# Optimization experiments

Measured on AMD Instinct MI355X. Metric: run time of the kernel, lower is better.

Reference implementation:

```python
import jax, jax.numpy as jnp
import numpy as np

B, N, E0, F_IN, H, EMB, VEC, DPI = 1024, 256, 2048, 6, 32, 32, 26, 512


def setup_inputs() -> dict:
    key = jax.random.key(0)
    ks = jax.random.split(key, 16)
    # fixed urban scene graph, shared by every batch element, with self-loops
    src0 = jax.random.randint(ks[0], (E0,), 0, N, dtype=jnp.int32)
    dst0 = jax.random.randint(ks[1], (E0,), 0, N, dtype=jnp.int32)
    loops = jnp.arange(N, dtype=jnp.int32)
    src = jnp.concatenate([src0, loops])
    dst = jnp.concatenate([dst0, loops])

    s = 0.05
    return {
        "graph_feats": jax.random.normal(ks[2], (B, N, F_IN), jnp.float32),
        "vector": jax.random.normal(ks[3], (B, VEC), jnp.float32),
        "src": src,
        "dst": dst,
        "W1": jax.random.normal(ks[4], (F_IN, H), jnp.float32) * s,
        "b1": jnp.zeros((H,), jnp.float32),
        "W2": jax.random.normal(ks[5], (H, H), jnp.float32) * s,
        "b2": jnp.zeros((H,), jnp.float32),
        "W3": jax.random.normal(ks[6], (H, H), jnp.float32) * s,
        "b3": jnp.zeros((H,), jnp.float32),
        "W_emb": jax.random.normal(ks[7], (H, EMB), jnp.float32) * s,
        "b_emb": jnp.zeros((EMB,), jnp.float32),
        "W_pi": jax.random.normal(ks[8], (VEC + EMB, DPI), jnp.float32) * s,
        "b_pi": jnp.zeros((DPI,), jnp.float32),
        "W_vf": jax.random.normal(ks[9], (VEC + EMB, DPI), jnp.float32) * s,
        "b_vf": jnp.zeros((DPI,), jnp.float32),
    }


def _edge_norm(src, dst, n_nodes):
    # DGL GraphConv norm='both': out_deg(src)^-1/2 * in_deg(dst)^-1/2
    ones = jnp.ones(src.shape[0], jnp.float32)
    deg_out = jax.ops.segment_sum(ones, src, num_segments=n_nodes)
    deg_in = jax.ops.segment_sum(ones, dst, num_segments=n_nodes)
    inv_o = jnp.where(deg_out > 0, deg_out ** -0.5, 0.0)
    inv_i = jnp.where(deg_in > 0, deg_in ** -0.5, 0.0)
    return inv_o[src] * inv_i[dst]  # [E]


def _gconv(h, src, dst, norm, W, b):
    # h: [B, N, F]; symmetric-normalized aggregation then linear (DGL GraphConv)
    msg = h[:, src, :] * norm[None, :, None]          # [B, E, F]
    agg = jnp.zeros_like(h).at[:, dst, :].add(msg)     # [B, N, F]
    return agg @ W + b


def reference(graph_feats, vector, src, dst, W1, b1, W2, b2, W3, b3,
              W_emb, b_emb, W_pi, b_pi, W_vf, b_vf):
    n_nodes = graph_feats.shape[1]
    norm = _edge_norm(src, dst, n_nodes)
    h = jax.nn.relu(_gconv(graph_feats, src, dst, norm, W1, b1))
    h = jax.nn.relu(_gconv(h, src, dst, norm, W2, b2))
    h = jax.nn.relu(_gconv(h, src, dst, norm, W3, b3))  # three_layers=True
    hg = jnp.mean(h, axis=1)                 # dgl.mean_nodes -> [B, H]
    emb = hg @ W_emb + b_emb                 # [B, EMB]
    comb = jnp.concatenate([vector[:, :26], emb], axis=1)  # [B, 58]
    pi = jax.nn.relu(comb @ W_pi + b_pi)
    vf = jax.nn.relu(comb @ W_vf + b_vf)
    return pi, vf
```

## Files before the change

kernel.cpp:

```cpp
#include <hip/hip_runtime.h>
#include <hip/hip_fp16.h>

#define B_    1024
#define N_    256
#define E_    2304
#define EPT_  9
#define FIN_  6
#define VEC_  26
#define HSTR_ 40

typedef _Float16 half8 __attribute__((ext_vector_type(8)));
typedef float    f32x4 __attribute__((ext_vector_type(4)));

__global__ __launch_bounds__(256) void fused_kernel(
    const float* __restrict__ gf,
    const float* __restrict__ vec,
    const int* __restrict__ src, const int* __restrict__ dst,
    const float* __restrict__ W1, const float* __restrict__ b1,
    const float* __restrict__ W2, const float* __restrict__ b2,
    const float* __restrict__ W3, const float* __restrict__ b3,
    const float* __restrict__ We, const float* __restrict__ be,
    const float* __restrict__ Wpi, const float* __restrict__ bpi,
    const float* __restrict__ Wvf, const float* __restrict__ bvf,
    float2* __restrict__ out)
{
    __shared__ __align__(16) __half hbuf[N_ * HSTR_];
    __shared__ unsigned int packedE[E_];
    __shared__ float part[8 * 33];
    __shared__ float hgl[32];
    __shared__ float comb[VEC_ + 32];
    __shared__ int   wsum[4];

    const int t = threadIdx.x;
    const int b = blockIdx.x;
    const int lane = t & 63, wv = t >> 6;

    int*   deg_o  = (int*)hbuf;
    int*   deg_i  = (int*)hbuf + 256;
    int*   scanA  = (int*)hbuf + 512;
    int*   cursor = (int*)hbuf + 768;
    int*   perm   = (int*)hbuf + 1024;
    float* inv_o  = (float*)hbuf + 1280;
    float* inv_i  = (float*)hbuf + 1536;
    int*   bcnt   = (int*)hbuf + 1792;
    int*   boff   = (int*)hbuf + 1856;

    deg_o[t] = 0; deg_i[t] = 0;
    if (t < 64) bcnt[t] = 0;
    __syncthreads();

    int sB[EPT_], dB[EPT_];
#pragma unroll
    for (int i = 0; i < EPT_; ++i) { int e = t + 256 * i; sB[i] = src[e]; dB[i] = dst[e]; }
#pragma unroll
    for (int i = 0; i < EPT_; ++i) { atomicAdd(&deg_o[sB[i]], 1); atomicAdd(&deg_i[dB[i]], 1); }
    __syncthreads();

    const int dI = deg_i[t];
    {
        int dO = deg_o[t];
        inv_o[t] = dO > 0 ? rsqrtf((float)dO) : 0.f;
        inv_i[t] = dI > 0 ? rsqrtf((float)dI) : 0.f;
    }
    int x = dI;
#pragma unroll
    for (int d = 1; d < 64; d <<= 1) {
        int y = __shfl_up(x, d, 64);
        if (lane >= d) x += y;
    }
    if (lane == 63) wsum[wv] = x;
    const int bucket = dI > 63 ? 63 : dI;
    atomicAdd(&bcnt[bucket], 1);
    __syncthreads();

    {
        int prefix = 0;
#pragma unroll
        for (int w = 0; w < 3; ++w) if (w < wv) prefix += wsum[w];
        int incl = x + prefix;
        scanA[t]  = incl;
        cursor[t] = incl - dI;
    }
    if (t < 64) {
        int c = bcnt[t], xx = c;
#pragma unroll
        for (int d = 1; d < 64; d <<= 1) {
            int y = __shfl_up(xx, d, 64);
            if (lane >= d) xx += y;
        }
        boff[t] = xx - c;
    }
    __syncthreads();

    { int pos = atomicAdd(&boff[bucket], 1); perm[pos] = t; }
#pragma unroll
    for (int i = 0; i < EPT_; ++i) {
        int s = sB[i], dd = dB[i];
        int pos = atomicAdd(&cursor[dd], 1);
        float nrm = inv_o[s] * inv_i[dd];
        unsigned short h = __half_as_ushort(__float2half(nrm));
        packedE[pos] = ((unsigned int)s << 16) | (unsigned int)h;
    }
    __syncthreads();

    const int node = perm[t];
    const int end  = scanA[node];
    const int beg  = end - deg_i[node];
    __syncthreads();

    {
        const float* g = gf + (size_t)b * (N_ * FIN_);
        for (int i = t; i < N_ * 8; i += 256) {
            int n = i >> 3, k = i & 7;
            hbuf[n * HSTR_ + k] = __float2half((k < FIN_) ? g[n * FIN_ + k] : 0.f);
        }
    }
    __syncthreads();

    const __half2 z2 = __float2half2_rn(0.f);

    {
        __half2 a2[4] = {z2, z2, z2, z2};
        for (int e = beg; e < end; ++e) {
            unsigned int u = packedE[e];
            __half2 w2 = __half2half2(__ushort_as_half((unsigned short)(u & 0xffffu)));
            union { float4 f4; __half2 h2[4]; } r;
            r.f4 = *(const float4*)&hbuf[(u >> 16) * HSTR_];
#pragma unroll
            for (int q = 0; q < 4; ++q) a2[q] = __hfma2(w2, r.h2[q], a2[q]);
        }
        float a[FIN_], o[32];
#pragma unroll
        for (int k = 0; k < FIN_; ++k)
            a[k] = (k & 1) ? __high2float(a2[k >> 1]) : __low2float(a2[k >> 1]);
#pragma unroll
        for (int j = 0; j < 32; ++j) o[j] = b1[j];
#pragma unroll
        for (int k = 0; k < FIN_; ++k) {
            float ak = a[k];
            const float* wr = &W1[k * 32];
#pragma unroll
            for (int j = 0; j < 32; ++j) o[j] += ak * wr[j];
        }
        __syncthreads();
        union { float4 f4; __half2 h2[4]; } w;
        float4* row = (float4*)&hbuf[node * HSTR_];
#pragma unroll
        for (int q = 0; q < 4; ++q) {
#pragma unroll
            for (int r = 0; r < 4; ++r)
                w.h2[r] = __floats2half2_rn(fmaxf(o[8*q + 2*r], 0.f), fmaxf(o[8*q + 2*r + 1], 0.f));
            row[q] = w.f4;
        }
    }
    __syncthreads();

    const int m16  = lane & 15;
    const int q4   = lane >> 4;
    const int slab = wv * 64;

    for (int L = 0; L < 2; ++L) {
        const float* Wl = (L == 0) ? W2 : W3;
        const float* Bl = (L == 0) ? b2 : b3;

        half8 bfrag[2];
        float bias_c[2];
#pragma unroll
        for (int h = 0; h < 2; ++h) {
            int col = m16 + 16 * h;
#pragma unroll
            for (int j = 0; j < 8; ++j)
                bfrag[h][j] = (_Float16)Wl[(q4 * 8 + j) * 32 + col];
            bias_c[h] = Bl[col];
        }

        __half2 acc2[16];
#pragma unroll
        for (int j = 0; j < 16; ++j) acc2[j] = z2;
        for (int e = beg; e < end; ++e) {
            unsigned int u = packedE[e];
            __half2 w2 = __half2half2(__ushort_as_half((unsigned short)(u & 0xffffu)));
            const float4* hr = (const float4*)&hbuf[(u >> 16) * HSTR_];
            union { float4 f4; __half2 h2[4]; } r0, r1, r2, r3;
            r0.f4 = hr[0]; r1.f4 = hr[1]; r2.f4 = hr[2]; r3.f4 = hr[3];
#pragma unroll
            for (int q = 0; q < 4; ++q) {
                acc2[q]      = __hfma2(w2, r0.h2[q], acc2[q]);
                acc2[4 + q]  = __hfma2(w2, r1.h2[q], acc2[4 + q]);
                acc2[8 + q]  = __hfma2(w2, r2.h2[q], acc2[8 + q]);
                acc2[12 + q] = __hfma2(w2, r3.h2[q], acc2[12 + q]);
            }
        }
        __syncthreads();
        {
            union { float4 f4; __half2 h2[4]; } w;
            float4* row = (float4*)&hbuf[node * HSTR_];
#pragma unroll
            for (int q = 0; q < 4; ++q) {
#pragma unroll
                for (int r = 0; r < 4; ++r) w.h2[r] = acc2[4 * q + r];
                row[q] = w.f4;
            }
        }
        __syncthreads();

        half8 afrag[4];
#pragma unroll
        for (int g = 0; g < 4; ++g) {
            union { float4 f4; half8 h8; } u;
            u.f4 = *(const float4*)&hbuf[(slab + g * 16 + m16) * HSTR_ + q4 * 8];
            afrag[g] = u.h8;
        }
        f32x4 D[4][2];
#pragma unroll
        for (int g = 0; g < 4; ++g) {
#pragma unroll
            for (int h = 0; h < 2; ++h) {
                f32x4 c = {bias_c[h], bias_c[h], bias_c[h], bias_c[h]};
                D[g][h] = __builtin_amdgcn_mfma_f32_16x16x32_f16(afrag[g], bfrag[h], c, 0, 0, 0);
            }
        }
#pragma unroll
        for (int g = 0; g < 4; ++g) {
#pragma unroll
            for (int h = 0; h < 2; ++h) {
#pragma unroll
                for (int r = 0; r < 4; ++r) {
                    float v = fmaxf(D[g][h][r], 0.f);
                    hbuf[(slab + g * 16 + q4 * 4 + r) * HSTR_ + h * 16 + m16] = __float2half(v);
                }
            }
        }
        __syncthreads();
    }

    {
        int j = t & 31, g8 = t >> 5;
        float s = 0.f;
        for (int i = 0; i < 32; ++i)
            s += __half2float(hbuf[(g8 * 32 + i) * HSTR_ + j]);
        part[g8 * 33 + j] = s;
    }
    __syncthreads();
    if (t < 32) {
        float sum = 0.f;
#pragma unroll
        for (int g8 = 0; g8 < 8; ++g8) sum += part[g8 * 33 + t];
        hgl[t] = sum * (1.0f / 256.0f);
    }
    __syncthreads();

    if (t < 32) {
        float v = be[t];
#pragma unroll
        for (int j = 0; j < 32; ++j) v += hgl[j] * We[j * 32 + t];
        comb[VEC_ + t] = v;
    }
    if (t < VEC_) comb[t] = vec[b * VEC_ + t];
    __syncthreads();

    {
        float p0 = bpi[2 * t], p1 = bpi[2 * t + 1];
        float v0 = bvf[2 * t], v1 = bvf[2 * t + 1];
        const float2* Wp = (const float2*)Wpi;
        const float2* Wv = (const float2*)Wvf;
        for (int k = 0; k < VEC_ + 32; ++k) {
            float c = comb[k];
            float2 a = Wp[k * 256 + t];
            p0 += c * a.x; p1 += c * a.y;
            float2 d = Wv[k * 256 + t];
            v0 += c * d.x; v1 += c * d.y;
        }
        out[b * 256 + t]          = make_float2(fmaxf(p0, 0.f), fmaxf(p1, 0.f));
        out[262144 + b * 256 + t] = make_float2(fmaxf(v0, 0.f), fmaxf(v1, 0.f));
    }
}

extern "C" void kernel_launch(void* const* d_in, const int* in_sizes, int n_in,
                              void* d_out, int out_size, void* d_ws, size_t ws_size,
                              hipStream_t stream)
{
    fused_kernel<<<B_, 256, 0, stream>>>(
        (const float*)d_in[0], (const float*)d_in[1],
        (const int*)d_in[2], (const int*)d_in[3],
        (const float*)d_in[4], (const float*)d_in[5],
        (const float*)d_in[6], (const float*)d_in[7],
        (const float*)d_in[8], (const float*)d_in[9],
        (const float*)d_in[10], (const float*)d_in[11],
        (const float*)d_in[12], (const float*)d_in[13],
        (const float*)d_in[14], (const float*)d_in[15],
        (float2*)d_out);
}
```

Before: 119.0 us.

## Split CSR build and MLP head into separate kernels around the GNN kernel

```diff
diff --git a/kernel.cpp b/kernel.cpp
--- a/kernel.cpp
+++ b/kernel.cpp
@@ -12,102 +12,109 @@
 typedef _Float16 half8 __attribute__((ext_vector_type(8)));
 typedef float    f32x4 __attribute__((ext_vector_type(4)));
 
+
+__global__ __launch_bounds__(256) void csr_kernel(
+    const int* __restrict__ src, const int* __restrict__ dst,
+    int4* __restrict__ nodeinfo, unsigned int* __restrict__ gpack)
+{
+    __shared__ int   deg_o[N_], deg_i[N_], scanA[N_], cursor[N_], perm[N_];
+    __shared__ float inv_o[N_], inv_i[N_];
+    __shared__ int   bcnt[64], boff[64], wsum[4];
+
+    const int t = threadIdx.x;
+    const int lane = t & 63, wv = t >> 6;
+
+    deg_o[t] = 0; deg_i[t] = 0;
+    if (t < 64) bcnt[t] = 0;
+    __syncthreads();
+
+    int sB[EPT_], dB[EPT_];
+#pragma unroll
+    for (int i = 0; i < EPT_; ++i) { int e = t + 256 * i; sB[i] = src[e]; dB[i] = dst[e]; }
+#pragma unroll
+    for (int i = 0; i < EPT_; ++i) { atomicAdd(&deg_o[sB[i]], 1); atomicAdd(&deg_i[dB[i]], 1); }
+    __syncthreads();
+
+    const int dI = deg_i[t];
+    {
+        int dO = deg_o[t];
+        inv_o[t] = dO > 0 ? rsqrtf((float)dO) : 0.f;
+        inv_i[t] = dI > 0 ? rsqrtf((float)dI) : 0.f;
+    }
+    int x = dI;
+#pragma unroll
+    for (int d = 1; d < 64; d <<= 1) {
+        int y = __shfl_up(x, d, 64);
+        if (lane >= d) x += y;
+    }
+    if (lane == 63) wsum[wv] = x;
+    const int bucket = dI > 63 ? 63 : dI;
+    atomicAdd(&bcnt[bucket], 1);
+    __syncthreads();
+
+    {
+        int prefix = 0;
+#pragma unroll
+        for (int w = 0; w < 3; ++w) if (w < wv) prefix += wsum[w];
+        int incl = x + prefix;
+        scanA[t]  = incl;
+        cursor[t] = incl - dI;
+    }
+    if (t < 64) {
+        int c = bcnt[t], xx = c;
+#pragma unroll
+        for (int d = 1; d < 64; d <<= 1) {
+            int y = __shfl_up(xx, d, 64);
+            if (lane >= d) xx += y;
+        }
+        boff[t] = xx - c;
+    }
+    __syncthreads();
+
+    { int pos = atomicAdd(&boff[bucket], 1); perm[pos] = t; }
+#pragma unroll
+    for (int i = 0; i < EPT_; ++i) {
+        int s = sB[i], dd = dB[i];
+        int pos = atomicAdd(&cursor[dd], 1);
+        float nrm = inv_o[s] * inv_i[dd];
+        unsigned short h = __half_as_ushort(__float2half(nrm));
+        gpack[pos] = ((unsigned int)s << 16) | (unsigned int)h;
+    }
+    __syncthreads();
+
+    {
+        int node = perm[t];
+        int end  = scanA[node];
+        int beg  = end - deg_i[node];
+        nodeinfo[t] = make_int4(node, beg, end, 0);
+    }
+}
+
 __global__ __launch_bounds__(256) void fused_kernel(
     const float* __restrict__ gf,
     const float* __restrict__ vec,
-    const int* __restrict__ src, const int* __restrict__ dst,
     const float* __restrict__ W1, const float* __restrict__ b1,
     const float* __restrict__ W2, const float* __restrict__ b2,
     const float* __restrict__ W3, const float* __restrict__ b3,
     const float* __restrict__ We, const float* __restrict__ be,
-    const float* __restrict__ Wpi, const float* __restrict__ bpi,
-    const float* __restrict__ Wvf, const float* __restrict__ bvf,
-    float2* __restrict__ out)
+    const int4* __restrict__ nodeinfo,
+    const unsigned int* __restrict__ gpack,
+    float* __restrict__ gcomb)
 {
     __shared__ __align__(16) __half hbuf[N_ * HSTR_];
     __shared__ unsigned int packedE[E_];
     __shared__ float part[8 * 33];
     __shared__ float hgl[32];
-    __shared__ float comb[VEC_ + 32];
-    __shared__ int   wsum[4];
 
     const int t = threadIdx.x;
     const int b = blockIdx.x;
-    const int lane = t & 63, wv = t >> 6;
-
-    int*   deg_o  = (int*)hbuf;
-    int*   deg_i  = (int*)hbuf + 256;
-    int*   scanA  = (int*)hbuf + 512;
-    int*   cursor = (int*)hbuf + 768;
-    int*   perm   = (int*)hbuf + 1024;
-    float* inv_o  = (float*)hbuf + 1280;
-    float* inv_i  = (float*)hbuf + 1536;
-    int*   bcnt   = (int*)hbuf + 1792;
-    int*   boff   = (int*)hbuf + 1856;
-
-    deg_o[t] = 0; deg_i[t] = 0;
-    if (t < 64) bcnt[t] = 0;
-    __syncthreads();
-
-    int sB[EPT_], dB[EPT_];
-#pragma unroll
-    for (int i = 0; i < EPT_; ++i) { int e = t + 256 * i; sB[i] = src[e]; dB[i] = dst[e]; }
-#pragma unroll
-    for (int i = 0; i < EPT_; ++i) { atomicAdd(&deg_o[sB[i]], 1); atomicAdd(&deg_i[dB[i]], 1); }
-    __syncthreads();
-
-    const int dI = deg_i[t];
-    {
-        int dO = deg_o[t];
-        inv_o[t] = dO > 0 ? rsqrtf((float)dO) : 0.f;
-        inv_i[t] = dI > 0 ? rsqrtf((float)dI) : 0.f;
-    }
-    int x = dI;
-#pragma unroll
-    for (int d = 1; d < 64; d <<= 1) {
-        int y = __shfl_up(x, d, 64);
-        if (lane >= d) x += y;
-    }
-    if (lane == 63) wsum[wv] = x;
-    const int bucket = dI > 63 ? 63 : dI;
-    atomicAdd(&bcnt[bucket], 1);
-    __syncthreads();
-
-    {
-        int prefix = 0;
-#pragma unroll
-        for (int w = 0; w < 3; ++w) if (w < wv) prefix += wsum[w];
-        int incl = x + prefix;
-        scanA[t]  = incl;
-        cursor[t] = incl - dI;
-    }
-    if (t < 64) {
-        int c = bcnt[t], xx = c;
-#pragma unroll
-        for (int d = 1; d < 64; d <<= 1) {
-            int y = __shfl_up(xx, d, 64);
-            if (lane >= d) xx += y;
-        }
-        boff[t] = xx - c;
-    }
-    __syncthreads();
-
-    { int pos = atomicAdd(&boff[bucket], 1); perm[pos] = t; }
-#pragma unroll
-    for (int i = 0; i < EPT_; ++i) {
-        int s = sB[i], dd = dB[i];
-        int pos = atomicAdd(&cursor[dd], 1);
-        float nrm = inv_o[s] * inv_i[dd];
-        unsigned short h = __half_as_ushort(__float2half(nrm));
-        packedE[pos] = ((unsigned int)s << 16) | (unsigned int)h;
-    }
-    __syncthreads();
-
-    const int node = perm[t];
-    const int end  = scanA[node];
-    const int beg  = end - deg_i[node];
-    __syncthreads();
-
+    const int lane = t & 63;
+
+    const int4 ni = nodeinfo[t];
+    const int node = ni.x, beg = ni.y, end = ni.z;
+
+#pragma unroll
+    for (int i = 0; i < EPT_; ++i) packedE[t + 256 * i] = gpack[t + 256 * i];
     {
         const float* g = gf + (size_t)b * (N_ * FIN_);
         for (int i = t; i < N_ * 8; i += 256) {
@@ -157,7 +164,7 @@
 
     const int m16  = lane & 15;
     const int q4   = lane >> 4;
-    const int slab = wv * 64;
+    const int slab = (t >> 6) * 64;
 
     for (int L = 0; L < 2; ++L) {
         const float* Wl = (L == 0) ? W2 : W3;
@@ -254,25 +261,46 @@
         float v = be[t];
 #pragma unroll
         for (int j = 0; j < 32; ++j) v += hgl[j] * We[j * 32 + t];
-        comb[VEC_ + t] = v;
-    }
-    if (t < VEC_) comb[t] = vec[b * VEC_ + t];
-    __syncthreads();
-
-    {
-        float p0 = bpi[2 * t], p1 = bpi[2 * t + 1];
-        float v0 = bvf[2 * t], v1 = bvf[2 * t + 1];
-        const float2* Wp = (const float2*)Wpi;
-        const float2* Wv = (const float2*)Wvf;
-        for (int k = 0; k < VEC_ + 32; ++k) {
-            float c = comb[k];
-            float2 a = Wp[k * 256 + t];
-            p0 += c * a.x; p1 += c * a.y;
-            float2 d = Wv[k * 256 + t];
-            v0 += c * d.x; v1 += c * d.y;
-        }
-        out[b * 256 + t]          = make_float2(fmaxf(p0, 0.f), fmaxf(p1, 0.f));
-        out[262144 + b * 256 + t] = make_float2(fmaxf(v0, 0.f), fmaxf(v1, 0.f));
+        gcomb[b * 64 + VEC_ + t] = v;
+    }
+    if (t < VEC_) gcomb[b * 64 + t] = vec[b * VEC_ + t];
+}
+
+__global__ __launch_bounds__(256) void head_kernel(
+    const float* __restrict__ gcomb,
+    const float* __restrict__ Wpi, const float* __restrict__ bpi,
+    const float* __restrict__ Wvf, const float* __restrict__ bvf,
+    float2* __restrict__ out)
+{
+    __shared__ float sc[4][64];
+    const int t = threadIdx.x;
+    const int b0 = blockIdx.x * 4;
+
+    { int i = t; sc[i >> 6][i & 63] = gcomb[b0 * 64 + i]; }
+    __syncthreads();
+
+    const float2 bp = ((const float2*)bpi)[t];
+    const float2 bv = ((const float2*)bvf)[t];
+    float2 accP[4] = {bp, bp, bp, bp};
+    float2 accV[4] = {bv, bv, bv, bv};
+
+    const float2* Wp = (const float2*)Wpi;
+    const float2* Wv = (const float2*)Wvf;
+    for (int k = 0; k < VEC_ + 32; ++k) {
+        float2 a = Wp[k * 256 + t];
+        float2 d = Wv[k * 256 + t];
+#pragma unroll
+        for (int b4 = 0; b4 < 4; ++b4) {
+            float c = sc[b4][k];
+            accP[b4].x += c * a.x; accP[b4].y += c * a.y;
+            accV[b4].x += c * d.x; accV[b4].y += c * d.y;
+        }
+    }
+#pragma unroll
+    for (int b4 = 0; b4 < 4; ++b4) {
+        int b = b0 + b4;
+        out[b * 256 + t]          = make_float2(fmaxf(accP[b4].x, 0.f), fmaxf(accP[b4].y, 0.f));
+        out[262144 + b * 256 + t] = make_float2(fmaxf(accV[b4].x, 0.f), fmaxf(accV[b4].y, 0.f));
     }
 }
 
@@ -280,13 +308,23 @@
                               void* d_out, int out_size, void* d_ws, size_t ws_size,
                               hipStream_t stream)
 {
+    int4*         nodeinfo = (int4*)d_ws;
+    unsigned int* gpack    = (unsigned int*)((char*)d_ws + 4096);
+    float*        gcomb    = (float*)((char*)d_ws + 16384);
+
+    csr_kernel<<<1, 256, 0, stream>>>(
+        (const int*)d_in[2], (const int*)d_in[3], nodeinfo, gpack);
+
     fused_kernel<<<B_, 256, 0, stream>>>(
         (const float*)d_in[0], (const float*)d_in[1],
-        (const int*)d_in[2], (const int*)d_in[3],
         (const float*)d_in[4], (const float*)d_in[5],
         (const float*)d_in[6], (const float*)d_in[7],
         (const float*)d_in[8], (const float*)d_in[9],
         (const float*)d_in[10], (const float*)d_in[11],
+        nodeinfo, gpack, gcomb);
+
+    head_kernel<<<256, 256, 0, stream>>>(
+        gcomb,
         (const float*)d_in[12], (const float*)d_in[13],
         (const float*)d_in[14], (const float*)d_in[15],
         (float2*)d_out);
```

Result: slower. 122.8 us (+3.2%).

## Process two batch elements per block to amortize graph preprocessing and weight loads

Applied to the files above, without the earlier changes.

```diff
diff --git a/kernel.cpp b/kernel.cpp
--- a/kernel.cpp
+++ b/kernel.cpp
@@ -8,6 +8,7 @@
 #define FIN_  6
 #define VEC_  26
 #define HSTR_ 40
+#define BPB_  2
 
 typedef _Float16 half8 __attribute__((ext_vector_type(8)));
 typedef float    f32x4 __attribute__((ext_vector_type(4)));
@@ -24,26 +25,26 @@
     const float* __restrict__ Wvf, const float* __restrict__ bvf,
     float2* __restrict__ out)
 {
-    __shared__ __align__(16) __half hbuf[N_ * HSTR_];
+    __shared__ __align__(16) __half hbuf[BPB_][N_ * HSTR_];
     __shared__ unsigned int packedE[E_];
-    __shared__ float part[8 * 33];
-    __shared__ float hgl[32];
-    __shared__ float comb[VEC_ + 32];
+    __shared__ float part[BPB_][8 * 33];
+    __shared__ float hgl[BPB_][32];
+    __shared__ float combS[BPB_][64];
     __shared__ int   wsum[4];
 
     const int t = threadIdx.x;
-    const int b = blockIdx.x;
+    const int b0 = blockIdx.x * BPB_;
     const int lane = t & 63, wv = t >> 6;
 
-    int*   deg_o  = (int*)hbuf;
-    int*   deg_i  = (int*)hbuf + 256;
-    int*   scanA  = (int*)hbuf + 512;
-    int*   cursor = (int*)hbuf + 768;
-    int*   perm   = (int*)hbuf + 1024;
-    float* inv_o  = (float*)hbuf + 1280;
-    float* inv_i  = (float*)hbuf + 1536;
-    int*   bcnt   = (int*)hbuf + 1792;
-    int*   boff   = (int*)hbuf + 1856;
+    int*   deg_o  = (int*)&hbuf[0][0];
+    int*   deg_i  = (int*)&hbuf[0][0] + 256;
+    int*   scanA  = (int*)&hbuf[0][0] + 512;
+    int*   cursor = (int*)&hbuf[0][0] + 768;
+    int*   perm   = (int*)&hbuf[0][0] + 1024;
+    float* inv_o  = (float*)&hbuf[0][0] + 1280;
+    float* inv_i  = (float*)&hbuf[0][0] + 1536;
+    int*   bcnt   = (int*)&hbuf[0][0] + 1792;
+    int*   boff   = (int*)&hbuf[0][0] + 1856;
 
     deg_o[t] = 0; deg_i[t] = 0;
     if (t < 64) bcnt[t] = 0;
@@ -109,10 +110,12 @@
     __syncthreads();
 
     {
-        const float* g = gf + (size_t)b * (N_ * FIN_);
+        const float* gA = gf + (size_t)b0 * (N_ * FIN_);
+        const float* gB = gA + N_ * FIN_;
         for (int i = t; i < N_ * 8; i += 256) {
             int n = i >> 3, k = i & 7;
-            hbuf[n * HSTR_ + k] = __float2half((k < FIN_) ? g[n * FIN_ + k] : 0.f);
+            hbuf[0][n * HSTR_ + k] = __float2half((k < FIN_) ? gA[n * FIN_ + k] : 0.f);
+            hbuf[1][n * HSTR_ + k] = __float2half((k < FIN_) ? gB[n * FIN_ + k] : 0.f);
         }
     }
     __syncthreads();
@@ -120,37 +123,46 @@
     const __half2 z2 = __float2half2_rn(0.f);
 
     {
-        __half2 a2[4] = {z2, z2, z2, z2};
+        __half2 aA[4] = {z2, z2, z2, z2};
+        __half2 aB[4] = {z2, z2, z2, z2};
         for (int e = beg; e < end; ++e) {
             unsigned int u = packedE[e];
             __half2 w2 = __half2half2(__ushort_as_half((unsigned short)(u & 0xffffu)));
-            union { float4 f4; __half2 h2[4]; } r;
-            r.f4 = *(const float4*)&hbuf[(u >> 16) * HSTR_];
-#pragma unroll
-            for (int q = 0; q < 4; ++q) a2[q] = __hfma2(w2, r.h2[q], a2[q]);
-        }
-        float a[FIN_], o[32];
-#pragma unroll
-        for (int k = 0; k < FIN_; ++k)
-            a[k] = (k & 1) ? __high2float(a2[k >> 1]) : __low2float(a2[k >> 1]);
-#pragma unroll
-        for (int j = 0; j < 32; ++j) o[j] = b1[j];
+            int ro = (u >> 16) * HSTR_;
+            union { float4 f4; __half2 h2[4]; } rA, rB;
+            rA.f4 = *(const float4*)&hbuf[0][ro];
+            rB.f4 = *(const float4*)&hbuf[1][ro];
+#pragma unroll
+            for (int q = 0; q < 4; ++q) {
+                aA[q] = __hfma2(w2, rA.h2[q], aA[q]);
+                aB[q] = __hfma2(w2, rB.h2[q], aB[q]);
+            }
+        }
+        float oA[32], oB[32];
+#pragma unroll
+        for (int j = 0; j < 32; ++j) { float bj = b1[j]; oA[j] = bj; oB[j] = bj; }
 #pragma unroll
         for (int k = 0; k < FIN_; ++k) {
-            float ak = a[k];
+            float akA = (k & 1) ? __high2float(aA[k >> 1]) : __low2float(aA[k >> 1]);
+            float akB = (k & 1) ? __high2float(aB[k >> 1]) : __low2float(aB[k >> 1]);
             const float* wr = &W1[k * 32];
 #pragma unroll
-            for (int j = 0; j < 32; ++j) o[j] += ak * wr[j];
+            for (int j = 0; j < 32; ++j) { float w = wr[j]; oA[j] += akA * w; oB[j] += akB * w; }
         }
         __syncthreads();
         union { float4 f4; __half2 h2[4]; } w;
-        float4* row = (float4*)&hbuf[node * HSTR_];
+        float4* rowA = (float4*)&hbuf[0][node * HSTR_];
+        float4* rowB = (float4*)&hbuf[1][node * HSTR_];
 #pragma unroll
         for (int q = 0; q < 4; ++q) {
 #pragma unroll
             for (int r = 0; r < 4; ++r)
-                w.h2[r] = __floats2half2_rn(fmaxf(o[8*q + 2*r], 0.f), fmaxf(o[8*q + 2*r + 1], 0.f));
-            row[q] = w.f4;
+                w.h2[r] = __floats2half2_rn(fmaxf(oA[8*q + 2*r], 0.f), fmaxf(oA[8*q + 2*r + 1], 0.f));
+            rowA[q] = w.f4;
+#pragma unroll
+            for (int r = 0; r < 4; ++r)
+                w.h2[r] = __floats2half2_rn(fmaxf(oB[8*q + 2*r], 0.f), fmaxf(oB[8*q + 2*r + 1], 0.f));
+            rowB[q] = w.f4;
         }
     }
     __syncthreads();
@@ -174,105 +186,137 @@
             bias_c[h] = Bl[col];
         }
 
-        __half2 acc2[16];
-#pragma unroll
-        for (int j = 0; j < 16; ++j) acc2[j] = z2;
+        __half2 accA[16], accB[16];
+#pragma unroll
+        for (int j = 0; j < 16; ++j) { accA[j] = z2; accB[j] = z2; }
         for (int e = beg; e < end; ++e) {
             unsigned int u = packedE[e];
             __half2 w2 = __half2half2(__ushort_as_half((unsigned short)(u & 0xffffu)));
-            const float4* hr = (const float4*)&hbuf[(u >> 16) * HSTR_];
+            int ro = (u >> 16) * HSTR_;
+            const float4* hrA = (const float4*)&hbuf[0][ro];
+            const float4* hrB = (const float4*)&hbuf[1][ro];
             union { float4 f4; __half2 h2[4]; } r0, r1, r2, r3;
-            r0.f4 = hr[0]; r1.f4 = hr[1]; r2.f4 = hr[2]; r3.f4 = hr[3];
+            r0.f4 = hrA[0]; r1.f4 = hrA[1]; r2.f4 = hrA[2]; r3.f4 = hrA[3];
 #pragma unroll
             for (int q = 0; q < 4; ++q) {
-                acc2[q]      = __hfma2(w2, r0.h2[q], acc2[q]);
-                acc2[4 + q]  = __hfma2(w2, r1.h2[q], acc2[4 + q]);
-                acc2[8 + q]  = __hfma2(w2, r2.h2[q], acc2[8 + q]);
-                acc2[12 + q] = __hfma2(w2, r3.h2[q], acc2[12 + q]);
+                accA[q]      = __hfma2(w2, r0.h2[q], accA[q]);
+                accA[4 + q]  = __hfma2(w2, r1.h2[q], accA[4 + q]);
+                accA[8 + q]  = __hfma2(w2, r2.h2[q], accA[8 + q]);
+                accA[12 + q] = __hfma2(w2, r3.h2[q], accA[12 + q]);
+            }
+            r0.f4 = hrB[0]; r1.f4 = hrB[1]; r2.f4 = hrB[2]; r3.f4 = hrB[3];
+#pragma unroll
+            for (int q = 0; q < 4; ++q) {
+                accB[q]      = __hfma2(w2, r0.h2[q], accB[q]);
+                accB[4 + q]  = __hfma2(w2, r1.h2[q], accB[4 + q]);
+                accB[8 + q]  = __hfma2(w2, r2.h2[q], accB[8 + q]);
+                accB[12 + q] = __hfma2(w2, r3.h2[q], accB[12 + q]);
             }
         }
         __syncthreads();
         {
             union { float4 f4; __half2 h2[4]; } w;
-            float4* row = (float4*)&hbuf[node * HSTR_];
+            float4* rowA = (float4*)&hbuf[0][node * HSTR_];
+            float4* rowB = (float4*)&hbuf[1][node * HSTR_];
 #pragma unroll
             for (int q = 0; q < 4; ++q) {
 #pragma unroll
-                for (int r = 0; r < 4; ++r) w.h2[r] = acc2[4 * q + r];
-                row[q] = w.f4;
+                for (int r = 0; r < 4; ++r) w.h2[r] = accA[4 * q + r];
+                rowA[q] = w.f4;
+#pragma unroll
+                for (int r = 0; r < 4; ++r) w.h2[r] = accB[4 * q + r];
+                rowB[q] = w.f4;
             }
         }
         __syncthreads();
 
-        half8 afrag[4];
-#pragma unroll
-        for (int g = 0; g < 4; ++g) {
-            union { float4 f4; half8 h8; } u;
-            u.f4 = *(const float4*)&hbuf[(slab + g * 16 + m16) * HSTR_ + q4 * 8];
-            afrag[g] = u.h8;
-        }
-        f32x4 D[4][2];
-#pragma unroll
-        for (int g = 0; g < 4; ++g) {
-#pragma unroll
-            for (int h = 0; h < 2; ++h) {
-                f32x4 c = {bias_c[h], bias_c[h], bias_c[h], bias_c[h]};
-                D[g][h] = __builtin_amdgcn_mfma_f32_16x16x32_f16(afrag[g], bfrag[h], c, 0, 0, 0);
-            }
-        }
-#pragma unroll
-        for (int g = 0; g < 4; ++g) {
-#pragma unroll
-            for (int h = 0; h < 2; ++h) {
-#pragma unroll
-                for (int r = 0; r < 4; ++r) {
-                    float v = fmaxf(D[g][h][r], 0.f);
-                    hbuf[(slab + g * 16 + q4 * 4 + r) * HSTR_ + h * 16 + m16] = __float2half(v);
+#pragma unroll
+        for (int bb = 0; bb < BPB_; ++bb) {
+            half8 afrag[4];
+#pragma unroll
+            for (int g = 0; g < 4; ++g) {
+                union { float4 f4; half8 h8; } u;
+                u.f4 = *(const float4*)&hbuf[bb][(slab + g * 16 + m16) * HSTR_ + q4 * 8];
+                afrag[g] = u.h8;
+            }
+            f32x4 D[4][2];
+#pragma unroll
+            for (int g = 0; g < 4; ++g) {
+#pragma unroll
+                for (int h = 0; h < 2; ++h) {
+                    f32x4 c = {bias_c[h], bias_c[h], bias_c[h], bias_c[h]};
+                    D[g][h] = __builtin_amdgcn_mfma_f32_16x16x32_f16(afrag[g], bfrag[h], c, 0, 0, 0);
                 }
             }
+#pragma unroll
+            for (int g = 0; g < 4; ++g) {
+#pragma unroll
+                for (int h = 0; h < 2; ++h) {
+#pragma unroll
+                    for (int r = 0; r < 4; ++r) {
+                        float v = fmaxf(D[g][h][r], 0.f);
+                        hbuf[bb][(slab + g * 16 + q4 * 4 + r) * HSTR_ + h * 16 + m16] = __float2half(v);
+                    }
+                }
+            }
         }
         __syncthreads();
     }
 
     {
         int j = t & 31, g8 = t >> 5;
-        float s = 0.f;
-        for (int i = 0; i < 32; ++i)
-            s += __half2float(hbuf[(g8 * 32 + i) * HSTR_ + j]);
-        part[g8 * 33 + j] = s;
-    }
-    __syncthreads();
-    if (t < 32) {
+        float sA = 0.f, sB = 0.f;
+        for (int i = 0; i < 32; ++i) {
+            int ro = (g8 * 32 + i) * HSTR_ + j;
+            sA += __half2float(hbuf[0][ro]);
+            sB += __half2float(hbuf[1][ro]);
+        }
+        part[0][g8 * 33 + j] = sA;
+        part[1][g8 * 33 + j] = sB;
+    }
+    __syncthreads();
+    if (t < 64) {
+        int bb = t >> 5, j = t & 31;
         float sum = 0.f;
 #pragma unroll
-        for (int g8 = 0; g8 < 8; ++g8) sum += part[g8 * 33 + t];
-        hgl[t] = sum * (1.0f / 256.0f);
-    }
-    __syncthreads();
-
-    if (t < 32) {
-        float v = be[t];
-#pragma unroll
-        for (int j = 0; j < 32; ++j) v += hgl[j] * We[j * 32 + t];
-        comb[VEC_ + t] = v;
-    }
-    if (t < VEC_) comb[t] = vec[b * VEC_ + t];
-    __syncthreads();
-
-    {
-        float p0 = bpi[2 * t], p1 = bpi[2 * t + 1];
-        float v0 = bvf[2 * t], v1 = bvf[2 * t + 1];
+        for (int g8 = 0; g8 < 8; ++g8) sum += part[bb][g8 * 33 + j];
+        hgl[bb][j] = sum * (1.0f / 256.0f);
+    }
+    if (t < BPB_ * VEC_) {
+        int bb = t / VEC_, j = t - bb * VEC_;
+        combS[bb][j] = vec[(b0 + bb) * VEC_ + j];
+    }
+    __syncthreads();
+
+    if (t < 64) {
+        int bb = t >> 5, j = t & 31;
+        float v = be[j];
+#pragma unroll
+        for (int k = 0; k < 32; ++k) v += hgl[bb][k] * We[k * 32 + j];
+        combS[bb][VEC_ + j] = v;
+    }
+    __syncthreads();
+
+    {
+        const float2 bp = ((const float2*)bpi)[t];
+        const float2 bv = ((const float2*)bvf)[t];
+        float2 aP0 = bp, aP1 = bp, aV0 = bv, aV1 = bv;
         const float2* Wp = (const float2*)Wpi;
         const float2* Wv = (const float2*)Wvf;
         for (int k = 0; k < VEC_ + 32; ++k) {
-            float c = comb[k];
             float2 a = Wp[k * 256 + t];
-            p0 += c * a.x; p1 += c * a.y;
             float2 d = Wv[k * 256 + t];
-            v0 += c * d.x; v1 += c * d.y;
-        }
-        out[b * 256 + t]          = make_float2(fmaxf(p0, 0.f), fmaxf(p1, 0.f));
-        out[262144 + b * 256 + t] = make_float2(fmaxf(v0, 0.f), fmaxf(v1, 0.f));
+            float c0 = combS[0][k];
+            float c1 = combS[1][k];
+            aP0.x += c0 * a.x; aP0.y += c0 * a.y;
+            aP1.x += c1 * a.x; aP1.y += c1 * a.y;
+            aV0.x += c0 * d.x; aV0.y += c0 * d.y;
+            aV1.x += c1 * d.x; aV1.y += c1 * d.y;
+        }
+        out[b0 * 256 + t]                = make_float2(fmaxf(aP0.x, 0.f), fmaxf(aP0.y, 0.f));
+        out[(b0 + 1) * 256 + t]          = make_float2(fmaxf(aP1.x, 0.f), fmaxf(aP1.y, 0.f));
+        out[262144 + b0 * 256 + t]       = make_float2(fmaxf(aV0.x, 0.f), fmaxf(aV0.y, 0.f));
+        out[262144 + (b0 + 1) * 256 + t] = make_float2(fmaxf(aV1.x, 0.f), fmaxf(aV1.y, 0.f));
     }
 }
 
@@ -280,7 +324,7 @@
                               void* d_out, int out_size, void* d_ws, size_t ws_size,
                               hipStream_t stream)
 {
-    fused_kernel<<<B_, 256, 0, stream>>>(
+    fused_kernel<<<B_ / BPB_, 256, 0, stream>>>(
         (const float*)d_in[0], (const float*)d_in[1],
         (const int*)d_in[2], (const int*)d_in[3],
         (const float*)d_in[4], (const float*)d_in[5],
```

Result: no change. 117.6 us (median of 2 runs) (-1.2%).

## Pad CSR edge lists to multiples of four and vectorize edge loads

Applied to the files above, without the earlier changes.

```diff
diff --git a/kernel.cpp b/kernel.cpp
--- a/kernel.cpp
+++ b/kernel.cpp
@@ -5,6 +5,7 @@
 #define N_    256
 #define E_    2304
 #define EPT_  9
+#define EP_   3072
 #define FIN_  6
 #define VEC_  26
 #define HSTR_ 40
@@ -12,7 +13,7 @@
 typedef _Float16 half8 __attribute__((ext_vector_type(8)));
 typedef float    f32x4 __attribute__((ext_vector_type(4)));
 
-__global__ __launch_bounds__(256) void fused_kernel(
+__global__ __launch_bounds__(256, 4) void fused_kernel(
     const float* __restrict__ gf,
     const float* __restrict__ vec,
     const int* __restrict__ src, const int* __restrict__ dst,
@@ -25,7 +26,7 @@
     float2* __restrict__ out)
 {
     __shared__ __align__(16) __half hbuf[N_ * HSTR_];
-    __shared__ unsigned int packedE[E_];
+    __shared__ __align__(16) unsigned int packedE[EP_];
     __shared__ float part[8 * 33];
     __shared__ float hgl[32];
     __shared__ float comb[VEC_ + 32];
@@ -34,6 +35,11 @@
     const int t = threadIdx.x;
     const int b = blockIdx.x;
     const int lane = t & 63, wv = t >> 6;
+
+    const float* gft = gf + (size_t)b * (N_ * FIN_) + t * FIN_;
+    const float2 f01 = *(const float2*)(gft);
+    const float2 f23 = *(const float2*)(gft + 2);
+    const float2 f45 = *(const float2*)(gft + 4);
 
     int*   deg_o  = (int*)hbuf;
     int*   deg_i  = (int*)hbuf + 256;
@@ -57,12 +63,13 @@
     __syncthreads();
 
     const int dI = deg_i[t];
+    const int dP = (dI + 3) & ~3;
     {
         int dO = deg_o[t];
         inv_o[t] = dO > 0 ? rsqrtf((float)dO) : 0.f;
         inv_i[t] = dI > 0 ? rsqrtf((float)dI) : 0.f;
     }
-    int x = dI;
+    int x = dP;
 #pragma unroll
     for (int d = 1; d < 64; d <<= 1) {
         int y = __shfl_up(x, d, 64);
@@ -79,7 +86,7 @@
         for (int w = 0; w < 3; ++w) if (w < wv) prefix += wsum[w];
         int incl = x + prefix;
         scanA[t]  = incl;
-        cursor[t] = incl - dI;
+        cursor[t] = incl - dP;
     }
     if (t < 64) {
         int c = bcnt[t], xx = c;
@@ -101,19 +108,25 @@
         unsigned short h = __half_as_ushort(__float2half(nrm));
         packedE[pos] = ((unsigned int)s << 16) | (unsigned int)h;
     }
+    {
+        int e0 = scanA[t] - dP + dI, e1 = scanA[t];
+        for (int p = e0; p < e1; ++p) packedE[p] = 0u;
+    }
     __syncthreads();
 
     const int node = perm[t];
+    const int dIn  = deg_i[node];
     const int end  = scanA[node];
-    const int beg  = end - deg_i[node];
-    __syncthreads();
-
-    {
-        const float* g = gf + (size_t)b * (N_ * FIN_);
-        for (int i = t; i < N_ * 8; i += 256) {
-            int n = i >> 3, k = i & 7;
-            hbuf[n * HSTR_ + k] = __float2half((k < FIN_) ? g[n * FIN_ + k] : 0.f);
-        }
+    const int beg  = end - ((dIn + 3) & ~3);
+    __syncthreads();
+
+    {
+        union { float4 f4; __half2 h2[4]; } w;
+        w.h2[0] = __floats2half2_rn(f01.x, f01.y);
+        w.h2[1] = __floats2half2_rn(f23.x, f23.y);
+        w.h2[2] = __floats2half2_rn(f45.x, f45.y);
+        w.h2[3] = __floats2half2_rn(0.f, 0.f);
+        *(float4*)&hbuf[t * HSTR_] = w.f4;
     }
     __syncthreads();
 
@@ -121,14 +134,20 @@
 
     {
         __half2 a2[4] = {z2, z2, z2, z2};
-        for (int e = beg; e < end; ++e) {
-            unsigned int u = packedE[e];
-            __half2 w2 = __half2half2(__ushort_as_half((unsigned short)(u & 0xffffu)));
-            union { float4 f4; __half2 h2[4]; } r;
-            r.f4 = *(const float4*)&hbuf[(u >> 16) * HSTR_];
-#pragma unroll
-            for (int q = 0; q < 4; ++q) a2[q] = __hfma2(w2, r.h2[q], a2[q]);
-        }
+#define L1_EDGE(U) { \
+        __half2 w2 = __half2half2(__ushort_as_half((unsigned short)((U) & 0xffffu))); \
+        union { float4 f4; __half2 h2[4]; } r; \
+        r.f4 = *(const float4*)&hbuf[((U) >> 16) * HSTR_]; \
+        a2[0] = __hfma2(w2, r.h2[0], a2[0]); a2[1] = __hfma2(w2, r.h2[1], a2[1]); \
+        a2[2] = __hfma2(w2, r.h2[2], a2[2]); a2[3] = __hfma2(w2, r.h2[3], a2[3]); }
+        uint4 uu = *(const uint4*)&packedE[beg];
+        for (int e = beg; e < end; e += 4) {
+            uint4 uun = uu;
+            if (e + 4 < end) uun = *(const uint4*)&packedE[e + 4];
+            L1_EDGE(uu.x); L1_EDGE(uu.y); L1_EDGE(uu.z); L1_EDGE(uu.w);
+            uu = uun;
+        }
+#undef L1_EDGE
         float a[FIN_], o[32];
 #pragma unroll
         for (int k = 0; k < FIN_; ++k)
@@ -177,20 +196,27 @@
         __half2 acc2[16];
 #pragma unroll
         for (int j = 0; j < 16; ++j) acc2[j] = z2;
-        for (int e = beg; e < end; ++e) {
-            unsigned int u = packedE[e];
-            __half2 w2 = __half2half2(__ushort_as_half((unsigned short)(u & 0xffffu)));
-            const float4* hr = (const float4*)&hbuf[(u >> 16) * HSTR_];
-            union { float4 f4; __half2 h2[4]; } r0, r1, r2, r3;
-            r0.f4 = hr[0]; r1.f4 = hr[1]; r2.f4 = hr[2]; r3.f4 = hr[3];
-#pragma unroll
-            for (int q = 0; q < 4; ++q) {
-                acc2[q]      = __hfma2(w2, r0.h2[q], acc2[q]);
-                acc2[4 + q]  = __hfma2(w2, r1.h2[q], acc2[4 + q]);
-                acc2[8 + q]  = __hfma2(w2, r2.h2[q], acc2[8 + q]);
-                acc2[12 + q] = __hfma2(w2, r3.h2[q], acc2[12 + q]);
-            }
-        }
+#define L23_EDGE(U) { \
+        __half2 w2 = __half2half2(__ushort_as_half((unsigned short)((U) & 0xffffu))); \
+        const float4* hr = (const float4*)&hbuf[((U) >> 16) * HSTR_]; \
+        union { float4 f4; __half2 h2[4]; } r0, r1, r2, r3; \
+        r0.f4 = hr[0]; r1.f4 = hr[1]; r2.f4 = hr[2]; r3.f4 = hr[3]; \
+        acc2[0]  = __hfma2(w2, r0.h2[0], acc2[0]);  acc2[1]  = __hfma2(w2, r0.h2[1], acc2[1]); \
+        acc2[2]  = __hfma2(w2, r0.h2[2], acc2[2]);  acc2[3]  = __hfma2(w2, r0.h2[3], acc2[3]); \
+        acc2[4]  = __hfma2(w2, r1.h2[0], acc2[4]);  acc2[5]  = __hfma2(w2, r1.h2[1], acc2[5]); \
+        acc2[6]  = __hfma2(w2, r1.h2[2], acc2[6]);  acc2[7]  = __hfma2(w2, r1.h2[3], acc2[7]); \
+        acc2[8]  = __hfma2(w2, r2.h2[0], acc2[8]);  acc2[9]  = __hfma2(w2, r2.h2[1], acc2[9]); \
+        acc2[10] = __hfma2(w2, r2.h2[2], acc2[10]); acc2[11] = __hfma2(w2, r2.h2[3], acc2[11]); \
+        acc2[12] = __hfma2(w2, r3.h2[0], acc2[12]); acc2[13] = __hfma2(w2, r3.h2[1], acc2[13]); \
+        acc2[14] = __hfma2(w2, r3.h2[2], acc2[14]); acc2[15] = __hfma2(w2, r3.h2[3], acc2[15]); }
+        uint4 uu = *(const uint4*)&packedE[beg];
+        for (int e = beg; e < end; e += 4) {
+            uint4 uun = uu;
+            if (e + 4 < end) uun = *(const uint4*)&packedE[e + 4];
+            L23_EDGE(uu.x); L23_EDGE(uu.y); L23_EDGE(uu.z); L23_EDGE(uu.w);
+            uu = uun;
+        }
+#undef L23_EDGE
         __syncthreads();
         {
             union { float4 f4; __half2 h2[4]; } w;
@@ -264,6 +290,7 @@
         float v0 = bvf[2 * t], v1 = bvf[2 * t + 1];
         const float2* Wp = (const float2*)Wpi;
         const float2* Wv = (const float2*)Wvf;
+#pragma unroll 2
         for (int k = 0; k < VEC_ + 32; ++k) {
             float c = comb[k];
             float2 a = Wp[k * 256 + t];
```

Measured after the change: 119.7 us. Within noise of the previous version (+0.6%).
